# Performance work log

Hardware: AMD Instinct MI355X
Metric: run time of the kernel (lower is better)

Reference implementation:

```python
import jax, jax.numpy as jnp
import numpy as np

E = 8
HIDDEN = 1024
INTER = 4096
CAPS = np.array([512, 1024, 2048, 4096, 1024, 512, 2048, 1024], dtype=np.int64)  # sum = 12288
TOTAL = int(CAPS.sum())


def setup_inputs() -> dict:
    key = jax.random.key(0)
    k1, k2, k3, k4, k5 = jax.random.split(key, 5)
    s1 = 1.0 / np.sqrt(HIDDEN)
    s2 = 1.0 / np.sqrt(INTER)
    return {
        "inter_state": jax.random.normal(k1, (TOTAL, HIDDEN), dtype=jnp.float32),
        "w1": jax.random.normal(k2, (E, INTER, HIDDEN), dtype=jnp.float32) * s1,
        "b1": jax.random.normal(k3, (E, INTER), dtype=jnp.float32) * s1,
        "w2": jax.random.normal(k4, (E, HIDDEN, INTER), dtype=jnp.float32) * s2,
        "b2": jax.random.normal(k5, (E, HIDDEN), dtype=jnp.float32) * s2,
        "capacities": jnp.asarray(CAPS),
    }


def reference(inter_state, w1, b1, w2, b2, capacities):
    # Grouped GEMM: tokens are contiguous per expert with sizes = capacities.
    # Capacities are routing metadata (static for slicing).
    caps = np.asarray(capacities)
    offs = np.concatenate([[0], np.cumsum(caps)]).astype(np.int64)
    outs = []
    for e in range(caps.shape[0]):  # small fixed expert loop
        x = inter_state[int(offs[e]):int(offs[e + 1])]      # [cap_e, hidden]
        h = x @ w1[e].T + b1[e]                              # [cap_e, inter]
        outs.append(h @ w2[e].T + b2[e])                     # [cap_e, hidden]
    return jnp.concatenate(outs, axis=0)                     # [total, hidden]
```

## Files before the change

kernel.cpp:

```cpp
#include <hip/hip_runtime.h>
#include <hip/hip_bf16.h>

#define DEV __device__ __forceinline__

typedef __bf16 bf16x8 __attribute__((ext_vector_type(8)));
typedef float  f32x4  __attribute__((ext_vector_type(4)));


DEV unsigned short f2bf(float f) {
  union { float f; unsigned u; } v; v.f = f;
  unsigned u = v.u;
  return (unsigned short)((u + 0x7FFFu + ((u >> 16) & 1u)) >> 16);
}

DEV int swz(int r, int cbyte) {
  return (r * 64 + cbyte) ^ (((r >> 1) & 7) << 4);
}

DEV void gld_lds16(const void* g, void* l) {
  __builtin_amdgcn_global_load_lds(
      (const __attribute__((address_space(1))) unsigned int*)g,
      (__attribute__((address_space(3))) unsigned int*)l, 16, 0, 0);
}

template <int K_, int N_, int NCT_, int AMODE, int BMODE, bool OUT_BF16,
          bool HAS_BIAS, int EDIV>
__global__ __launch_bounds__(256)
void gemm_expert(const void* __restrict__ Av, const void* __restrict__ Bv,
                 const float* __restrict__ bias, void* __restrict__ Cv) {
  __shared__ char lds[16384];
  char* As = lds;
  char* Bs = lds + 8192;

  const int t    = threadIdx.x;
  const int lane = t & 63;
  const int wv   = t >> 6;
  const int wr   = wv >> 1;
  const int wc   = wv & 1;
  const int fr   = lane & 15;
  const int fq   = lane >> 4;

  const int rt = blockIdx.x / NCT_;
  const int ct = blockIdx.x - rt * NCT_;

  int e;
  if constexpr (EDIV > 0) {
    e = rt / EDIV;
  } else {
    const int cums[9] = {0, 4, 12, 28, 60, 68, 72, 88, 96};
    e = 0;
#pragma unroll
    for (int i = 1; i < 8; ++i) e += (rt >= cums[i]) ? 1 : 0;
  }

  const int grow0 = rt * 128;
  const int nloc0 = ct * 128;

  f32x4 acc[4][4];
#pragma unroll
  for (int i = 0; i < 4; ++i)
#pragma unroll
    for (int j = 0; j < 4; ++j) acc[i][j] = (f32x4){0.f, 0.f, 0.f, 0.f};

  for (int kb = 0; kb < K_; kb += 32) {
    __syncthreads();
    if constexpr (AMODE == 1) {
      const unsigned short* Ab = (const unsigned short*)Av;
#pragma unroll
      for (int s = 0; s < 2; ++s) {
        int o = (wv * 2 + s) * 1024 + lane * 16;
        int p = o ^ (((o >> 7) & 7) << 4);
        const unsigned short* g =
            Ab + (size_t)(grow0 + (p >> 6)) * K_ + kb + ((p & 63) >> 1);
        gld_lds16(g, As + (wv * 2 + s) * 1024);
      }
    }
    if constexpr (BMODE == 1) {
      const unsigned short* Bb = (const unsigned short*)Bv + (size_t)e * N_ * K_;
#pragma unroll
      for (int s = 0; s < 2; ++s) {
        int o = (wv * 2 + s) * 1024 + lane * 16;
        int p = o ^ (((o >> 7) & 7) << 4);
        const unsigned short* g =
            Bb + (size_t)(nloc0 + (p >> 6)) * K_ + kb + ((p & 63) >> 1);
        gld_lds16(g, Bs + (wv * 2 + s) * 1024);
      }
    }
    if constexpr (AMODE == 0) {
      const float* Af = (const float*)Av;
#pragma unroll
      for (int it = 0; it < 4; ++it) {
        int q = t + it * 256, r = q >> 3, c = (q & 7) * 4;
        float4 f = *(const float4*)(Af + (size_t)(grow0 + r) * K_ + kb + c);
        ushort4 v = {f2bf(f.x), f2bf(f.y), f2bf(f.z), f2bf(f.w)};
        *(ushort4*)(As + swz(r, c * 2)) = v;
      }
    }
    if constexpr (BMODE == 0) {
      const float* Bf = (const float*)Bv + (size_t)e * N_ * K_;
#pragma unroll
      for (int it = 0; it < 4; ++it) {
        int q = t + it * 256, r = q >> 3, c = (q & 7) * 4;
        float4 f = *(const float4*)(Bf + (size_t)(nloc0 + r) * K_ + kb + c);
        ushort4 v = {f2bf(f.x), f2bf(f.y), f2bf(f.z), f2bf(f.w)};
        *(ushort4*)(Bs + swz(r, c * 2)) = v;
      }
    }
    __syncthreads();

    bf16x8 af[4], bfg[4];
#pragma unroll
    for (int mi = 0; mi < 4; ++mi)
      af[mi] = *(bf16x8*)(As + swz(wr * 64 + mi * 16 + fr, fq * 16));
#pragma unroll
    for (int ni = 0; ni < 4; ++ni)
      bfg[ni] = *(bf16x8*)(Bs + swz(wc * 64 + ni * 16 + fr, fq * 16));
#pragma unroll
    for (int mi = 0; mi < 4; ++mi)
#pragma unroll
      for (int ni = 0; ni < 4; ++ni)
        acc[mi][ni] = __builtin_amdgcn_mfma_f32_16x16x32_bf16(
            af[mi], bfg[ni], acc[mi][ni], 0, 0, 0);
  }

#pragma unroll
  for (int ni = 0; ni < 4; ++ni) {
    int nloc = nloc0 + wc * 64 + ni * 16 + fr;
    float bv = 0.f;
    if constexpr (HAS_BIAS) bv = (bias + (size_t)e * N_)[nloc];
#pragma unroll
    for (int mi = 0; mi < 4; ++mi) {
      int m = grow0 + wr * 64 + mi * 16 + fq * 4;
#pragma unroll
      for (int j = 0; j < 4; ++j) {
        float val = acc[mi][ni][j] + bv;
        if constexpr (OUT_BF16)
          ((unsigned short*)Cv)[(size_t)(m + j) * N_ + nloc] = f2bf(val);
        else
          ((float*)Cv)[(size_t)(m + j) * N_ + nloc] = val;
      }
    }
  }
}

__global__ __launch_bounds__(256)
void transpose_w1(const float* __restrict__ w1, unsigned short* __restrict__ w1t) {
  __shared__ unsigned short tl[64 * 68];
  int b = blockIdx.x;
  int jt = b & 15, kt = (b >> 4) & 63, e = b >> 10;
  const float* src = w1 + ((size_t)e * 4096 + kt * 64) * 1024 + jt * 64;
  int t = threadIdx.x;
#pragma unroll
  for (int it = 0; it < 4; ++it) {
    int q = t + it * 256, kr = q >> 4, jc = (q & 15) * 4;
    float4 f = *(const float4*)(src + (size_t)kr * 1024 + jc);
    ushort4 v = {f2bf(f.x), f2bf(f.y), f2bf(f.z), f2bf(f.w)};
    *(ushort4*)&tl[kr * 68 + jc] = v;
  }
  __syncthreads();
  unsigned short* dst = w1t + ((size_t)e * 1024 + jt * 64) * 4096 + kt * 64;
#pragma unroll
  for (int it = 0; it < 4; ++it) {
    int q = t + it * 256, jr = q >> 4, kc = (q & 15) * 4;
    ushort4 v = {tl[(kc + 0) * 68 + jr], tl[(kc + 1) * 68 + jr],
                 tl[(kc + 2) * 68 + jr], tl[(kc + 3) * 68 + jr]};
    *(ushort4*)(dst + (size_t)jr * 4096 + kc) = v;
  }
}

template <bool STORE_BF>
__global__ __launch_bounds__(256)
void conv_w2_bias(const float* __restrict__ w2, const float* __restrict__ b1,
                  const float* __restrict__ b2, unsigned short* __restrict__ w2bf,
                  float* __restrict__ bc) {
  int row = blockIdx.x, e = row >> 10, t = threadIdx.x;
  const float* src = w2 + (size_t)row * 4096;
  const float* b1e = b1 + (size_t)e * 4096;
  float acc = 0.f;
#pragma unroll
  for (int it = 0; it < 4; ++it) {
    int c = (t + it * 256) * 4;
    float4 f = *(const float4*)(src + c);
    float4 g = *(const float4*)(b1e + c);
    acc += f.x * g.x + f.y * g.y + f.z * g.z + f.w * g.w;
    if constexpr (STORE_BF) {
      ushort4 v = {f2bf(f.x), f2bf(f.y), f2bf(f.z), f2bf(f.w)};
      *(ushort4*)(w2bf + (size_t)row * 4096 + c) = v;
    }
  }
#pragma unroll
  for (int o = 32; o > 0; o >>= 1) acc += __shfl_down(acc, o);
  __shared__ float red[4];
  if ((t & 63) == 0) red[t >> 6] = acc;
  __syncthreads();
  if (t == 0) bc[row] = red[0] + red[1] + red[2] + red[3] + b2[row];
}

__global__ __launch_bounds__(256)
void conv_f32_bf16(const float* __restrict__ in, unsigned short* __restrict__ out,
                   int n4) {
  for (int i = blockIdx.x * 256 + threadIdx.x; i < n4; i += gridDim.x * 256) {
    float4 f = *(const float4*)(in + (size_t)i * 4);
    ushort4 v = {f2bf(f.x), f2bf(f.y), f2bf(f.z), f2bf(f.w)};
    *(ushort4*)(out + (size_t)i * 4) = v;
  }
}

extern "C" void kernel_launch(void* const* d_in, const int* in_sizes, int n_in,
                              void* d_out, int out_size, void* d_ws, size_t ws_size,
                              hipStream_t stream) {
  const float* x  = (const float*)d_in[0];
  const float* w1 = (const float*)d_in[1];
  const float* b1 = (const float*)d_in[2];
  const float* w2 = (const float*)d_in[3];
  const float* b2 = (const float*)d_in[4];

  char* ws = (char*)d_ws;
  unsigned short* w1t = (unsigned short*)ws;
  const size_t NEED_T2 = 151126016, NEED_T3 = 176291840;

  if (ws_size >= NEED_T2) {
    unsigned short* w2bf = (unsigned short*)(ws + 67108864);
    unsigned short* Wc   = (unsigned short*)(ws + 134217728);
    float*          bc   = (float*)(ws + 150994944);

    transpose_w1<<<8192, 256, 0, stream>>>(w1, w1t);
    conv_w2_bias<true><<<8192, 256, 0, stream>>>(w2, b1, b2, w2bf, bc);
    gemm_expert<4096, 1024, 8, 1, 1, true, false, 8>
        <<<512, 256, 0, stream>>>(w2bf, w1t, nullptr, Wc);
    if (ws_size >= NEED_T3) {
      unsigned short* xbf = (unsigned short*)(ws + 151126016);
      conv_f32_bf16<<<2048, 256, 0, stream>>>(x, xbf, 12288 * 1024 / 4);
      gemm_expert<1024, 1024, 8, 1, 1, false, true, 0>
          <<<768, 256, 0, stream>>>(xbf, Wc, bc, d_out);
    } else {
      gemm_expert<1024, 1024, 8, 0, 1, false, true, 0>
          <<<768, 256, 0, stream>>>(x, Wc, bc, d_out);
    }
  } else {
    unsigned short* Wc = (unsigned short*)(ws + 67108864);
    float*          bc = (float*)(ws + 83886080);

    transpose_w1<<<8192, 256, 0, stream>>>(w1, w1t);
    conv_w2_bias<false><<<8192, 256, 0, stream>>>(w2, b1, b2, nullptr, bc);
    gemm_expert<4096, 1024, 8, 0, 1, true, false, 8>
        <<<512, 256, 0, stream>>>(w2, w1t, nullptr, Wc);
    gemm_expert<1024, 1024, 8, 0, 1, false, true, 0>
        <<<768, 256, 0, stream>>>(x, Wc, bc, d_out);
  }
}
```

Baseline: 250.7 us.

## Double-buffer LDS in expert GEMM, halve N tile, and remap block order

```diff
diff --git a/kernel.cpp b/kernel.cpp
--- a/kernel.cpp
+++ b/kernel.cpp
@@ -28,9 +28,7 @@
 __global__ __launch_bounds__(256)
 void gemm_expert(const void* __restrict__ Av, const void* __restrict__ Bv,
                  const float* __restrict__ bias, void* __restrict__ Cv) {
-  __shared__ char lds[16384];
-  char* As = lds;
-  char* Bs = lds + 8192;
+  __shared__ char lds[2][12288];
 
   const int t    = threadIdx.x;
   const int lane = t & 63;
@@ -40,8 +38,12 @@
   const int fr   = lane & 15;
   const int fq   = lane >> 4;
 
-  const int rt = blockIdx.x / NCT_;
-  const int ct = blockIdx.x - rt * NCT_;
+  int bid = blockIdx.x;
+  const int nwg = gridDim.x;
+  if ((nwg & 7) == 0) bid = (bid & 7) * (nwg >> 3) + (bid >> 3);
+
+  const int rt = bid / NCT_;
+  const int ct = bid - rt * NCT_;
 
   int e;
   if constexpr (EDIV > 0) {
@@ -54,40 +56,31 @@
   }
 
   const int grow0 = rt * 128;
-  const int nloc0 = ct * 128;
-
-  f32x4 acc[4][4];
+  const int nloc0 = ct * 64;
+
+  f32x4 acc[4][2];
 #pragma unroll
   for (int i = 0; i < 4; ++i)
 #pragma unroll
-    for (int j = 0; j < 4; ++j) acc[i][j] = (f32x4){0.f, 0.f, 0.f, 0.f};
-
-  for (int kb = 0; kb < K_; kb += 32) {
-    __syncthreads();
+    for (int j = 0; j < 2; ++j) acc[i][j] = (f32x4){0.f, 0.f, 0.f, 0.f};
+
+  const unsigned short* Ab = (const unsigned short*)Av;
+  const float*          Af = (const float*)Av;
+  const unsigned short* Bb = (const unsigned short*)Bv + (size_t)e * N_ * K_;
+  const float*          Bf = (const float*)Bv + (size_t)e * N_ * K_;
+
+  auto stage = [&](int buf, int kb) {
+    char* As = lds[buf];
+    char* Bs = lds[buf] + 8192;
     if constexpr (AMODE == 1) {
-      const unsigned short* Ab = (const unsigned short*)Av;
 #pragma unroll
       for (int s = 0; s < 2; ++s) {
         int o = (wv * 2 + s) * 1024 + lane * 16;
         int p = o ^ (((o >> 7) & 7) << 4);
-        const unsigned short* g =
-            Ab + (size_t)(grow0 + (p >> 6)) * K_ + kb + ((p & 63) >> 1);
-        gld_lds16(g, As + (wv * 2 + s) * 1024);
-      }
-    }
-    if constexpr (BMODE == 1) {
-      const unsigned short* Bb = (const unsigned short*)Bv + (size_t)e * N_ * K_;
-#pragma unroll
-      for (int s = 0; s < 2; ++s) {
-        int o = (wv * 2 + s) * 1024 + lane * 16;
-        int p = o ^ (((o >> 7) & 7) << 4);
-        const unsigned short* g =
-            Bb + (size_t)(nloc0 + (p >> 6)) * K_ + kb + ((p & 63) >> 1);
-        gld_lds16(g, Bs + (wv * 2 + s) * 1024);
-      }
-    }
-    if constexpr (AMODE == 0) {
-      const float* Af = (const float*)Av;
+        gld_lds16(Ab + (size_t)(grow0 + (p >> 6)) * K_ + kb + ((p & 63) >> 1),
+                  As + (wv * 2 + s) * 1024);
+      }
+    } else {
 #pragma unroll
       for (int it = 0; it < 4; ++it) {
         int q = t + it * 256, r = q >> 3, c = (q & 7) * 4;
@@ -96,36 +89,55 @@
         *(ushort4*)(As + swz(r, c * 2)) = v;
       }
     }
-    if constexpr (BMODE == 0) {
-      const float* Bf = (const float*)Bv + (size_t)e * N_ * K_;
-#pragma unroll
-      for (int it = 0; it < 4; ++it) {
+    if constexpr (BMODE == 1) {
+      int o = wv * 1024 + lane * 16;
+      int p = o ^ (((o >> 7) & 7) << 4);
+      gld_lds16(Bb + (size_t)(nloc0 + (p >> 6)) * K_ + kb + ((p & 63) >> 1),
+                Bs + wv * 1024);
+    } else {
+#pragma unroll
+      for (int it = 0; it < 2; ++it) {
         int q = t + it * 256, r = q >> 3, c = (q & 7) * 4;
         float4 f = *(const float4*)(Bf + (size_t)(nloc0 + r) * K_ + kb + c);
         ushort4 v = {f2bf(f.x), f2bf(f.y), f2bf(f.z), f2bf(f.w)};
         *(ushort4*)(Bs + swz(r, c * 2)) = v;
       }
     }
-    __syncthreads();
-
-    bf16x8 af[4], bfg[4];
+  };
+
+  auto compute = [&](int buf) {
+    char* As = lds[buf];
+    char* Bs = lds[buf] + 8192;
+    bf16x8 af[4], bfg[2];
 #pragma unroll
     for (int mi = 0; mi < 4; ++mi)
       af[mi] = *(bf16x8*)(As + swz(wr * 64 + mi * 16 + fr, fq * 16));
 #pragma unroll
-    for (int ni = 0; ni < 4; ++ni)
-      bfg[ni] = *(bf16x8*)(Bs + swz(wc * 64 + ni * 16 + fr, fq * 16));
+    for (int ni = 0; ni < 2; ++ni)
+      bfg[ni] = *(bf16x8*)(Bs + swz(wc * 32 + ni * 16 + fr, fq * 16));
 #pragma unroll
     for (int mi = 0; mi < 4; ++mi)
 #pragma unroll
-      for (int ni = 0; ni < 4; ++ni)
+      for (int ni = 0; ni < 2; ++ni)
         acc[mi][ni] = __builtin_amdgcn_mfma_f32_16x16x32_bf16(
             af[mi], bfg[ni], acc[mi][ni], 0, 0, 0);
-  }
-
-#pragma unroll
-  for (int ni = 0; ni < 4; ++ni) {
-    int nloc = nloc0 + wc * 64 + ni * 16 + fr;
+  };
+
+  int cur = 0;
+  stage(0, 0);
+  __syncthreads();
+#pragma unroll 2
+  for (int kb = 32; kb < K_; kb += 32) {
+    stage(cur ^ 1, kb);
+    compute(cur);
+    __syncthreads();
+    cur ^= 1;
+  }
+  compute(cur);
+
+#pragma unroll
+  for (int ni = 0; ni < 2; ++ni) {
+    int nloc = nloc0 + wc * 32 + ni * 16 + fr;
     float bv = 0.f;
     if constexpr (HAS_BIAS) bv = (bias + (size_t)e * N_)[nloc];
 #pragma unroll
@@ -226,16 +238,16 @@
 
     transpose_w1<<<8192, 256, 0, stream>>>(w1, w1t);
     conv_w2_bias<true><<<8192, 256, 0, stream>>>(w2, b1, b2, w2bf, bc);
-    gemm_expert<4096, 1024, 8, 1, 1, true, false, 8>
-        <<<512, 256, 0, stream>>>(w2bf, w1t, nullptr, Wc);
+    gemm_expert<4096, 1024, 16, 1, 1, true, false, 8>
+        <<<1024, 256, 0, stream>>>(w2bf, w1t, nullptr, Wc);
     if (ws_size >= NEED_T3) {
       unsigned short* xbf = (unsigned short*)(ws + 151126016);
       conv_f32_bf16<<<2048, 256, 0, stream>>>(x, xbf, 12288 * 1024 / 4);
-      gemm_expert<1024, 1024, 8, 1, 1, false, true, 0>
-          <<<768, 256, 0, stream>>>(xbf, Wc, bc, d_out);
+      gemm_expert<1024, 1024, 16, 1, 1, false, true, 0>
+          <<<1536, 256, 0, stream>>>(xbf, Wc, bc, d_out);
     } else {
-      gemm_expert<1024, 1024, 8, 0, 1, false, true, 0>
-          <<<768, 256, 0, stream>>>(x, Wc, bc, d_out);
+      gemm_expert<1024, 1024, 16, 0, 1, false, true, 0>
+          <<<1536, 256, 0, stream>>>(x, Wc, bc, d_out);
     }
   } else {
     unsigned short* Wc = (unsigned short*)(ws + 67108864);
@@ -243,9 +255,9 @@
 
     transpose_w1<<<8192, 256, 0, stream>>>(w1, w1t);
     conv_w2_bias<false><<<8192, 256, 0, stream>>>(w2, b1, b2, nullptr, bc);
-    gemm_expert<4096, 1024, 8, 0, 1, true, false, 8>
-        <<<512, 256, 0, stream>>>(w2, w1t, nullptr, Wc);
-    gemm_expert<1024, 1024, 8, 0, 1, false, true, 0>
-        <<<768, 256, 0, stream>>>(x, Wc, bc, d_out);
-  }
-}
+    gemm_expert<4096, 1024, 16, 0, 1, true, false, 8>
+        <<<1024, 256, 0, stream>>>(w2, w1t, nullptr, Wc);
+    gemm_expert<1024, 1024, 16, 0, 1, false, true, 0>
+        <<<1536, 256, 0, stream>>>(x, Wc, bc, d_out);
+  }
+}
```

After: 240.0 us. 4.3% less time.
